# Kernel tuning notes

Measured on AMD Instinct MI355X. Metric: run time of the kernel, lower is better.

## Reference

```python
import jax, jax.numpy as jnp
import numpy as np

NUM_HEADS = 8
B, L, D = 4, 1024, 512


def sinusoidal_embeddings(length, dim, decay_term=10000.0):
    positions = jnp.arange(1 - length, length, dtype=jnp.float32).reshape(-1, 1)
    div_term = jnp.exp(-jnp.arange(0, dim, 2, dtype=jnp.float32) * (np.log(decay_term) / dim))
    return jnp.concatenate([jnp.sin(positions * div_term), jnp.cos(positions * div_term)], axis=1)


def setup_inputs() -> dict:
    key = jax.random.key(0)
    k1, k2 = jax.random.split(key)
    x = jax.random.normal(k1, (B, L, D), dtype=jnp.float32)
    W = jax.random.normal(k2, (D, 3 * D), dtype=jnp.float32) * 0.02
    b = jnp.zeros((3 * D,), dtype=jnp.float32)
    return {"x": x, "W": W, "b": b}


def reference(x, W, b):
    batch, length, dim = x.shape
    d_head = dim // NUM_HEADS
    # pointwise Conv(3*dim, kernel_size=1) == dense projection
    proj = jnp.einsum('bld,de->ble', x, W) + b  # [B, L, 3*dim]
    # split heads exactly as the module: reshape to [B,L,H,3*d_head], move heads, split into q,k,v
    proj = proj.reshape(batch, length, NUM_HEADS, 3 * d_head).transpose(0, 2, 1, 3)
    q, k, v = jnp.split(proj, 3, axis=3)  # each [B, H, L, d_head]
    qk = jnp.einsum('bhqd,bhkd->bhqk', q, k)
    # relative position scores via gather (unoptimized path)
    emb_matrix = sinusoidal_embeddings(length, d_head)  # [2L-1, d_head]
    indices = jnp.arange(length)[:, None] - jnp.arange(length) + length - 1  # [L, L]
    embeddings = emb_matrix[indices]  # [L, L, d_head]
    qe = jnp.einsum('bhqd,qkd->bhqk', q, embeddings)
    weights = jax.nn.softmax((qk + qe) / jnp.sqrt(jnp.float32(d_head)), axis=-1)
    output = jnp.einsum('bhqk,bhkd->bhqd', weights, v)
    return output.transpose(0, 2, 1, 3).reshape(batch, length, dim)
```

## Files before the change

kernel.cpp:

```cpp
#include <hip/hip_runtime.h>

typedef unsigned short UST;
typedef __attribute__((ext_vector_type(8))) __bf16 bf16x8;
typedef __attribute__((ext_vector_type(4))) float f32x4;
typedef __attribute__((ext_vector_type(16))) float f32x16;

#define NB 4
#define NH 8
#define LSEQ 1024
#define DMODEL 512
#define DH 64

__device__ __forceinline__ UST f2bf(float f) {
  union { float f; unsigned u; } v; v.f = f;
  unsigned u = v.u;
  return (UST)((u + 0x7FFFu + ((u >> 16) & 1u)) >> 16);
}
__device__ __forceinline__ float bf2f(UST h) {
  union { unsigned u; float f; } v; v.u = ((unsigned)h) << 16;
  return v.f;
}
__device__ __forceinline__ unsigned cvt_pk_bf16(float lo, float hi) {
  unsigned r;
  asm volatile("v_cvt_pk_bf16_f32 %0, %1, %2" : "=v"(r) : "v"(lo), "v"(hi));
  return r;
}

__global__ void k_convert_x(const float* __restrict__ x, UST* __restrict__ xbf) {
  int i = blockIdx.x * 256 + threadIdx.x;
  float4 v = ((const float4*)x)[i];
  ushort4 o;
  o.x = f2bf(v.x); o.y = f2bf(v.y); o.z = f2bf(v.z); o.w = f2bf(v.w);
  ((ushort4*)xbf)[i] = o;
}

__global__ void k_transpose_W(const float* __restrict__ W, UST* __restrict__ WT) {
  __shared__ float tile[64][65];
  int n0 = blockIdx.x * 64;
  int k0 = blockIdx.y * 64;
  int tx = threadIdx.x & 63, ty = threadIdx.x >> 6;
#pragma unroll
  for (int i = 0; i < 16; ++i) {
    int k = ty + i * 4;
    tile[k][tx] = W[(size_t)(k0 + k) * 1536 + n0 + tx];
  }
  __syncthreads();
#pragma unroll
  for (int i = 0; i < 16; ++i) {
    int n = ty + i * 4;
    WT[(size_t)(n0 + n) * 512 + k0 + tx] = f2bf(tile[tx][n]);
  }
}

__global__ __launch_bounds__(256) void k_proj(
    const UST* __restrict__ xbf, const UST* __restrict__ WT, const float* __restrict__ bias,
    UST* __restrict__ qext, UST* __restrict__ kext, UST* __restrict__ vT) {
  int m0 = blockIdx.x * 128;
  int n0 = blockIdx.y * 64;
  int t = threadIdx.x;
  int lane = t & 63, w = t >> 6;
  int wr = w >> 1, wc = w & 1;
  int g = lane >> 4, c16 = lane & 15;

  __shared__ UST AtS[128 * 64];
  __shared__ UST BtS[64 * 64];

  const char* Ag = (const char*)(xbf + (size_t)m0 * 512);
  const char* Bg = (const char*)(WT + (size_t)n0 * 512);

  bf16x8 areg[4], breg[2];
#pragma unroll
  for (int c = 0; c < 4; ++c) {
    int u = c * 256 + t, r = u >> 3, s = u & 7;
    areg[c] = *(const bf16x8*)(Ag + (size_t)r * 1024 + s * 16);
  }
#pragma unroll
  for (int c = 0; c < 2; ++c) {
    int u = c * 256 + t, r = u >> 3, s = u & 7;
    breg[c] = *(const bf16x8*)(Bg + (size_t)r * 1024 + s * 16);
  }

  f32x4 acc[4][2] = {};
  for (int kk = 0; kk < 512; kk += 64) {
    __syncthreads();
#pragma unroll
    for (int c = 0; c < 4; ++c) {
      int u = c * 256 + t, r = u >> 3, s = u & 7;
      *(bf16x8*)((char*)AtS + (size_t)r * 128 + (s ^ (r & 7)) * 16) = areg[c];
    }
#pragma unroll
    for (int c = 0; c < 2; ++c) {
      int u = c * 256 + t, r = u >> 3, s = u & 7;
      *(bf16x8*)((char*)BtS + (size_t)r * 128 + (s ^ (r & 7)) * 16) = breg[c];
    }
    __syncthreads();

    if (kk + 64 < 512) {
      size_t cb = (size_t)(kk + 64) * 2;
#pragma unroll
      for (int c = 0; c < 4; ++c) {
        int u = c * 256 + t, r = u >> 3, s = u & 7;
        areg[c] = *(const bf16x8*)(Ag + (size_t)r * 1024 + cb + s * 16);
      }
#pragma unroll
      for (int c = 0; c < 2; ++c) {
        int u = c * 256 + t, r = u >> 3, s = u & 7;
        breg[c] = *(const bf16x8*)(Bg + (size_t)r * 1024 + cb + s * 16);
      }
    }

#pragma unroll
    for (int kf = 0; kf < 2; ++kf) {
      bf16x8 af[4], bfr[2];
#pragma unroll
      for (int rf = 0; rf < 4; ++rf) {
        int r = wr * 64 + rf * 16 + c16;
        int s = (kf * 4 + g) ^ (r & 7);
        af[rf] = *(const bf16x8*)((const char*)AtS + (size_t)r * 128 + s * 16);
      }
#pragma unroll
      for (int cf = 0; cf < 2; ++cf) {
        int r = wc * 32 + cf * 16 + c16;
        int s = (kf * 4 + g) ^ (r & 7);
        bfr[cf] = *(const bf16x8*)((const char*)BtS + (size_t)r * 128 + s * 16);
      }
      __builtin_amdgcn_s_setprio(1);
#pragma unroll
      for (int rf = 0; rf < 4; ++rf)
#pragma unroll
        for (int cf = 0; cf < 2; ++cf)
          acc[rf][cf] = __builtin_amdgcn_mfma_f32_16x16x32_bf16(af[rf], bfr[cf], acc[rf][cf], 0, 0, 0);
      __builtin_amdgcn_s_setprio(0);
    }
  }

#pragma unroll
  for (int rf = 0; rf < 4; ++rf) {
#pragma unroll
    for (int cf = 0; cf < 2; ++cf) {
      int c = n0 + wc * 32 + cf * 16 + c16;
      int h = c / 192, rem = c % 192;
      float bv = bias[c];
#pragma unroll
      for (int r = 0; r < 4; ++r) {
        int row = m0 + wr * 64 + rf * 16 + g * 4 + r;
        int bidx = row >> 10, ltok = row & 1023;
        int bh = bidx * 8 + h;
        float val = acc[rf][cf][r] + bv;
        if (rem < 64)
          qext[((size_t)bh * 1024 + ltok) * 128 + rem] = f2bf(val * 0.125f);
        else if (rem < 128)
          kext[((size_t)bh * 1024 + ltok) * 128 + (rem - 64)] = f2bf(val);
        else
          vT[((size_t)bh * 64 + (rem - 128)) * 1024 + ltok] = f2bf(val);
      }
    }
  }
}

__global__ void k_relpos(UST* __restrict__ qext, UST* __restrict__ kext) {
  int gid = blockIdx.x * 256 + threadIdx.x;
  int j = gid & 31;
  int l = (gid >> 5) & 1023;
  int bh = gid >> 15;
  float dd = exp2f((float)(-2 * j) * 0.20762050593046f);
  float ang = (float)l * dd;
  float s = __sinf(ang), c = __cosf(ang);
  UST* qp = qext + ((size_t)bh * 1024 + l) * 128;
  float qs = bf2f(qp[j]), qc = bf2f(qp[32 + j]);
  qp[64 + j] = f2bf(qs * s + qc * c);
  qp[96 + j] = f2bf(qc * s - qs * c);
  UST* kp = kext + ((size_t)bh * 1024 + l) * 128;
  kp[64 + j] = f2bf(c);
  kp[96 + j] = f2bf(s);
}

template<int SPLITS>
__global__ __launch_bounds__(256) void k_attn_split(
    const UST* __restrict__ qext, const UST* __restrict__ kext,
    const UST* __restrict__ vT,
    float* __restrict__ Opart, float* __restrict__ ml) {
  int blk = ((blockIdx.x & 7) << 6) | (blockIdx.x >> 3);
  int split = blockIdx.y;
  int qt = blk & 15, bh = blk >> 4;
  int q0 = qt * 64;
  int t = threadIdx.x;
  int lane = t & 63, w = t >> 6;
  int l31 = lane & 31, lh = lane >> 5;
  int wq = w >> 1, wk = w & 1;

  __shared__ UST KtS[64 * 128];
  __shared__ UST VtS[64 * 64];

  const UST* qbase = qext + ((size_t)bh * 1024 + q0 + wq * 32 + l31) * 128 + lh * 8;
  bf16x8 qf[8];
#pragma unroll
  for (int c = 0; c < 8; ++c) qf[c] = *(const bf16x8*)&qbase[c * 16];

  const char* kgbase = (const char*)(kext + (size_t)bh * 1024 * 128);
  const char* vgbase = (const char*)(vT + (size_t)bh * 64 * 1024);

  f32x16 O[2] = {};
  float l_lane = 0.f;

  int kbeg = split * (LSEQ / SPLITS);
  int kend = kbeg + LSEQ / SPLITS;

  bf16x8 kreg[4], vreg[2];
  {
    const char* kg = kgbase + (size_t)kbeg * 256;
#pragma unroll
    for (int c = 0; c < 4; ++c) {
      int u = c * 256 + t;
      kreg[c] = *(const bf16x8*)(kg + (size_t)(u >> 4) * 256 + (u & 15) * 16);
    }
    const char* vg = vgbase + (size_t)kbeg * 2;
#pragma unroll
    for (int c = 0; c < 2; ++c) {
      int u = c * 256 + t;
      vreg[c] = *(const bf16x8*)(vg + (size_t)(u >> 3) * 2048 + (u & 7) * 16);
    }
  }

  int krow = wk * 32 + l31;

  for (int k0 = kbeg; k0 < kend; k0 += 64) {
    __syncthreads();
#pragma unroll
    for (int c = 0; c < 4; ++c) {
      int u = c * 256 + t, r = u >> 4, s = u & 15;
      *(bf16x8*)((char*)KtS + (size_t)r * 256 + (s ^ (r & 7)) * 16) = kreg[c];
    }
#pragma unroll
    for (int c = 0; c < 2; ++c) {
      int u = c * 256 + t, r = u >> 3, s = u & 7;
      *(bf16x8*)((char*)VtS + (size_t)r * 128 + (s ^ (r & 7)) * 16) = vreg[c];
    }
    __syncthreads();

    if (k0 + 64 < kend) {
      const char* kg = kgbase + (size_t)(k0 + 64) * 256;
#pragma unroll
      for (int c = 0; c < 4; ++c) {
        int u = c * 256 + t;
        kreg[c] = *(const bf16x8*)(kg + (size_t)(u >> 4) * 256 + (u & 15) * 16);
      }
      const char* vg = vgbase + (size_t)(k0 + 64) * 2;
#pragma unroll
      for (int c = 0; c < 2; ++c) {
        int u = c * 256 + t;
        vreg[c] = *(const bf16x8*)(vg + (size_t)(u >> 3) * 2048 + (u & 7) * 16);
      }
    }

    f32x16 sa = {};
#pragma unroll
    for (int kh = 0; kh < 2; ++kh) {
      bf16x8 kfr[4];
#pragma unroll
      for (int kc = 0; kc < 4; ++kc) {
        int slot = ((kh * 4 + kc) * 2 + lh) ^ (krow & 7);
        kfr[kc] = *(const bf16x8*)((const char*)KtS + (size_t)krow * 256 + slot * 16);
      }
      __builtin_amdgcn_s_setprio(1);
#pragma unroll
      for (int kc = 0; kc < 4; ++kc)
        sa = __builtin_amdgcn_mfma_f32_32x32x16_bf16(kfr[kc], qf[kh * 4 + kc], sa, 0, 0, 0);
      __builtin_amdgcn_s_setprio(0);
    }

    float p[16];
#pragma unroll
    for (int i = 0; i < 16; ++i) {
      p[i] = __expf(sa[i]);
      l_lane += p[i];
    }
    unsigned wv[8], xv[8];
#pragma unroll
    for (int j = 0; j < 8; ++j) wv[j] = cvt_pk_bf16(p[2 * j], p[2 * j + 1]);
#pragma unroll
    for (int j = 0; j < 8; ++j) xv[j] = __shfl_xor((int)wv[j], 32, 64);
    int4 pa0i = lh ? (int4){(int)xv[2], (int)xv[3], (int)wv[2], (int)wv[3]}
                   : (int4){(int)wv[0], (int)wv[1], (int)xv[0], (int)xv[1]};
    int4 pa1i = lh ? (int4){(int)xv[6], (int)xv[7], (int)wv[6], (int)wv[7]}
                   : (int4){(int)wv[4], (int)wv[5], (int)xv[4], (int)xv[5]};
    bf16x8 pa[2] = {*(bf16x8*)&pa0i, *(bf16x8*)&pa1i};

#pragma unroll
    for (int dn = 0; dn < 2; ++dn) {
      int d = dn * 32 + l31;
      bf16x8 vf[2];
#pragma unroll
      for (int kc = 0; kc < 2; ++kc) {
        int slot = (wk * 4 + kc * 2 + lh) ^ (d & 7);
        vf[kc] = *(const bf16x8*)((const char*)VtS + (size_t)d * 128 + slot * 16);
      }
      __builtin_amdgcn_s_setprio(1);
#pragma unroll
      for (int kc = 0; kc < 2; ++kc)
        O[dn] = __builtin_amdgcn_mfma_f32_32x32x16_bf16(pa[kc], vf[kc], O[dn], 0, 0, 0);
      __builtin_amdgcn_s_setprio(0);
    }
  }

  l_lane += __shfl_xor(l_lane, 32, 64);
  int sp = split * 2 + wk;
  if (lh == 0) {
    float* mp = ml + (((size_t)sp * 32 + bh) * 1024 + q0 + wq * 32 + l31) * 2;
    mp[0] = 0.f;
    mp[1] = l_lane;
  }
#pragma unroll
  for (int i = 0; i < 16; ++i) {
    int qrow = q0 + wq * 32 + (i & 3) + 8 * (i >> 2) + 4 * lh;
    float* op = Opart + (((size_t)sp * 32 + bh) * 1024 + qrow) * 64 + l31;
    op[0] = O[0][i];
    op[32] = O[1][i];
  }
}

template<int PARTS>
__global__ void k_combine(const float* __restrict__ Opart, const float* __restrict__ ml,
                          float* __restrict__ out) {
  int gid = blockIdx.x * 256 + threadIdx.x;
  int dq = (gid & 15) * 4;
  int row = (gid >> 4) & 1023;
  int bh = gid >> 14;
  int b = bh >> 3, h = bh & 7;

  float denom = 0.f;
  float4 acc = {0.f, 0.f, 0.f, 0.f};
#pragma unroll
  for (int s = 0; s < PARTS; ++s) {
    denom += ml[(((size_t)s * 32 + bh) * 1024 + row) * 2 + 1];
    float4 ov = *(const float4*)&Opart[(((size_t)s * 32 + bh) * 1024 + row) * 64 + dq];
    acc.x += ov.x; acc.y += ov.y; acc.z += ov.z; acc.w += ov.w;
  }
  float inv = 1.0f / denom;
  float4 o = {acc.x * inv, acc.y * inv, acc.z * inv, acc.w * inv};
  *(float4*)&out[((size_t)b * 1024 + row) * 512 + h * 64 + dq] = o;
}

extern "C" void kernel_launch(void* const* d_in, const int* in_sizes, int n_in,
                              void* d_out, int out_size, void* d_ws, size_t ws_size,
                              hipStream_t stream) {
  const float* x = (const float*)d_in[0];
  const float* W = (const float*)d_in[1];
  const float* bias = (const float*)d_in[2];
  float* out = (float*)d_out;

  UST* ws = (UST*)d_ws;
  UST* xbf  = ws;
  UST* WT   = xbf + 4096 * 512;
  UST* qext = WT + 1536 * 512;
  UST* kext = qext + 32 * 1024 * 128;
  UST* vT   = kext + 32 * 1024 * 128;
  UST* bf_end = vT + 32 * 64 * 1024;

  size_t base_bytes = (size_t)(bf_end - ws) * sizeof(UST);
  size_t per_part = (size_t)32 * 1024 * 66 * sizeof(float);
  int S = 1;
  if (ws_size >= base_bytes + 4 * per_part) S = 2;

  float* Opart = (float*)bf_end;
  float* ml = Opart + (size_t)(2 * S) * 32 * 1024 * 64;

  k_convert_x<<<dim3(2048), dim3(256), 0, stream>>>(x, xbf);
  k_transpose_W<<<dim3(24, 8), dim3(256), 0, stream>>>(W, WT);
  k_proj<<<dim3(32, 24), dim3(256), 0, stream>>>(xbf, WT, bias, qext, kext, vT);
  k_relpos<<<dim3(4096), dim3(256), 0, stream>>>(qext, kext);

  if (S == 2) {
    k_attn_split<2><<<dim3(512, 2), dim3(256), 0, stream>>>(qext, kext, vT, Opart, ml);
    k_combine<4><<<dim3(2048), dim3(256), 0, stream>>>(Opart, ml, out);
  } else {
    k_attn_split<1><<<dim3(512, 1), dim3(256), 0, stream>>>(qext, kext, vT, Opart, ml);
    k_combine<2><<<dim3(2048), dim3(256), 0, stream>>>(Opart, ml, out);
  }
}
```

Baseline: 67.54 us.

## Drop split-K attention and fuse the partial-sum combine into the attention kernel

The attention kernel now processes the full key range per block instead of splitting it across two blocks. The two key-half wavefronts in each block merge their partial outputs and row sums through shared memory, reusing the K tile buffer as scratch. Each block then writes the normalized result straight to the output. This removes the float partial-output buffers, their global write and read-back, and the separate combine launch. In exchange the grid is halved to 512 blocks and each block runs a longer serial key loop, so there is less parallelism to hide latency.

Result: faster. 59.20 us (-12.3%).

```diff
diff --git a/kernel.cpp b/kernel.cpp
--- a/kernel.cpp
+++ b/kernel.cpp
@@ -175,14 +175,12 @@
   kp[96 + j] = f2bf(s);
 }
 
-template<int SPLITS>
-__global__ __launch_bounds__(256) void k_attn_split(
+__global__ __launch_bounds__(256) void k_attn(
     const UST* __restrict__ qext, const UST* __restrict__ kext,
-    const UST* __restrict__ vT,
-    float* __restrict__ Opart, float* __restrict__ ml) {
+    const UST* __restrict__ vT, float* __restrict__ out) {
   int blk = ((blockIdx.x & 7) << 6) | (blockIdx.x >> 3);
-  int split = blockIdx.y;
   int qt = blk & 15, bh = blk >> 4;
+  int b = bh >> 3, h = bh & 7;
   int q0 = qt * 64;
   int t = threadIdx.x;
   int lane = t & 63, w = t >> 6;
@@ -191,6 +189,7 @@
 
   __shared__ UST KtS[64 * 128];
   __shared__ UST VtS[64 * 64];
+  __shared__ float Lsum[2][2][32];
 
   const UST* qbase = qext + ((size_t)bh * 1024 + q0 + wq * 32 + l31) * 128 + lh * 8;
   bf16x8 qf[8];
@@ -203,18 +202,15 @@
   f32x16 O[2] = {};
   float l_lane = 0.f;
 
-  int kbeg = split * (LSEQ / SPLITS);
-  int kend = kbeg + LSEQ / SPLITS;
-
   bf16x8 kreg[4], vreg[2];
   {
-    const char* kg = kgbase + (size_t)kbeg * 256;
+    const char* kg = kgbase;
 #pragma unroll
     for (int c = 0; c < 4; ++c) {
       int u = c * 256 + t;
       kreg[c] = *(const bf16x8*)(kg + (size_t)(u >> 4) * 256 + (u & 15) * 16);
     }
-    const char* vg = vgbase + (size_t)kbeg * 2;
+    const char* vg = vgbase;
 #pragma unroll
     for (int c = 0; c < 2; ++c) {
       int u = c * 256 + t;
@@ -224,7 +220,7 @@
 
   int krow = wk * 32 + l31;
 
-  for (int k0 = kbeg; k0 < kend; k0 += 64) {
+  for (int k0 = 0; k0 < LSEQ; k0 += 64) {
     __syncthreads();
 #pragma unroll
     for (int c = 0; c < 4; ++c) {
@@ -238,7 +234,7 @@
     }
     __syncthreads();
 
-    if (k0 + 64 < kend) {
+    if (k0 + 64 < LSEQ) {
       const char* kg = kgbase + (size_t)(k0 + 64) * 256;
 #pragma unroll
       for (int c = 0; c < 4; ++c) {
@@ -279,7 +275,7 @@
 #pragma unroll
     for (int j = 0; j < 8; ++j) wv[j] = cvt_pk_bf16(p[2 * j], p[2 * j + 1]);
 #pragma unroll
-    for (int j = 0; j < 8; ++j) xv[j] = __shfl_xor((int)wv[j], 32, 64);
+    for (int j = 0; j < 8; ++j) xv[j] = (unsigned)__shfl_xor((int)wv[j], 32, 64);
     int4 pa0i = lh ? (int4){(int)xv[2], (int)xv[3], (int)wv[2], (int)wv[3]}
                    : (int4){(int)wv[0], (int)wv[1], (int)xv[0], (int)xv[1]};
     int4 pa1i = lh ? (int4){(int)xv[6], (int)xv[7], (int)wv[6], (int)wv[7]}
@@ -304,41 +300,29 @@
   }
 
   l_lane += __shfl_xor(l_lane, 32, 64);
-  int sp = split * 2 + wk;
-  if (lh == 0) {
-    float* mp = ml + (((size_t)sp * 32 + bh) * 1024 + q0 + wq * 32 + l31) * 2;
-    mp[0] = 0.f;
-    mp[1] = l_lane;
-  }
-#pragma unroll
-  for (int i = 0; i < 16; ++i) {
-    int qrow = q0 + wq * 32 + (i & 3) + 8 * (i >> 2) + 4 * lh;
-    float* op = Opart + (((size_t)sp * 32 + bh) * 1024 + qrow) * 64 + l31;
-    op[0] = O[0][i];
-    op[32] = O[1][i];
-  }
-}
-
-template<int PARTS>
-__global__ void k_combine(const float* __restrict__ Opart, const float* __restrict__ ml,
-                          float* __restrict__ out) {
-  int gid = blockIdx.x * 256 + threadIdx.x;
-  int dq = (gid & 15) * 4;
-  int row = (gid >> 4) & 1023;
-  int bh = gid >> 14;
-  int b = bh >> 3, h = bh & 7;
-
-  float denom = 0.f;
-  float4 acc = {0.f, 0.f, 0.f, 0.f};
-#pragma unroll
-  for (int s = 0; s < PARTS; ++s) {
-    denom += ml[(((size_t)s * 32 + bh) * 1024 + row) * 2 + 1];
-    float4 ov = *(const float4*)&Opart[(((size_t)s * 32 + bh) * 1024 + row) * 64 + dq];
-    acc.x += ov.x; acc.y += ov.y; acc.z += ov.z; acc.w += ov.w;
-  }
-  float inv = 1.0f / denom;
-  float4 o = {acc.x * inv, acc.y * inv, acc.z * inv, acc.w * inv};
-  *(float4*)&out[((size_t)b * 1024 + row) * 512 + h * 64 + dq] = o;
+  if (lh == 0) Lsum[wk][wq][l31] = l_lane;
+  __syncthreads();
+  float* scratch = (float*)KtS;
+  if (wk == 1) {
+#pragma unroll
+    for (int i = 0; i < 16; ++i) {
+      int qr = wq * 32 + ((i & 3) + 8 * (i >> 2) + 4 * lh);
+      scratch[qr * 64 + l31] = O[0][i];
+      scratch[qr * 64 + 32 + l31] = O[1][i];
+    }
+  }
+  __syncthreads();
+  if (wk == 0) {
+#pragma unroll
+    for (int i = 0; i < 16; ++i) {
+      int cr = (i & 3) + 8 * (i >> 2) + 4 * lh;
+      int qr = wq * 32 + cr;
+      float inv = 1.0f / (Lsum[0][wq][cr] + Lsum[1][wq][cr]);
+      float* op = out + ((size_t)b * 1024 + q0 + qr) * 512 + h * 64;
+      op[l31] = (O[0][i] + scratch[qr * 64 + l31]) * inv;
+      op[32 + l31] = (O[1][i] + scratch[qr * 64 + 32 + l31]) * inv;
+    }
+  }
 }
 
 extern "C" void kernel_launch(void* const* d_in, const int* in_sizes, int n_in,
@@ -355,26 +339,10 @@
   UST* qext = WT + 1536 * 512;
   UST* kext = qext + 32 * 1024 * 128;
   UST* vT   = kext + 32 * 1024 * 128;
-  UST* bf_end = vT + 32 * 64 * 1024;
-
-  size_t base_bytes = (size_t)(bf_end - ws) * sizeof(UST);
-  size_t per_part = (size_t)32 * 1024 * 66 * sizeof(float);
-  int S = 1;
-  if (ws_size >= base_bytes + 4 * per_part) S = 2;
-
-  float* Opart = (float*)bf_end;
-  float* ml = Opart + (size_t)(2 * S) * 32 * 1024 * 64;
 
   k_convert_x<<<dim3(2048), dim3(256), 0, stream>>>(x, xbf);
   k_transpose_W<<<dim3(24, 8), dim3(256), 0, stream>>>(W, WT);
   k_proj<<<dim3(32, 24), dim3(256), 0, stream>>>(xbf, WT, bias, qext, kext, vT);
   k_relpos<<<dim3(4096), dim3(256), 0, stream>>>(qext, kext);
-
-  if (S == 2) {
-    k_attn_split<2><<<dim3(512, 2), dim3(256), 0, stream>>>(qext, kext, vT, Opart, ml);
-    k_combine<4><<<dim3(2048), dim3(256), 0, stream>>>(Opart, ml, out);
-  } else {
-    k_attn_split<1><<<dim3(512, 1), dim3(256), 0, stream>>>(qext, kext, vT, Opart, ml);
-    k_combine<2><<<dim3(2048), dim3(256), 0, stream>>>(Opart, ml, out);
-  }
-}
+  k_attn<<<dim3(512), dim3(256), 0, stream>>>(qext, kext, vT, out);
+}
```
